# Optimization experiments

Hardware: AMD Instinct MI355X
Metric: run time of the kernel (lower is better)

The kernel has to match this reference:

```python
import jax, jax.numpy as jnp
import numpy as np

HEADS = 4
DIM_HEAD = 32
TOPK_RATIO = 0.25
MIN_TOPK = 32
QKEEP_RATIO = 0.75
MIN_QKEEP = 64
LN_EPS = 1e-5


def _ln(x, g, b):
    m = x.mean(-1, keepdims=True)
    v = x.var(-1, keepdims=True)  # biased, matches torch LayerNorm
    return (x - m) / jnp.sqrt(v + LN_EPS) * g + b


def setup_inputs() -> dict:
    key = jax.random.key(0)
    ks = jax.random.split(key, 8)
    b, n, x, y, w, d = 4, 4, 8, 8, 8, 128
    hd = HEADS * DIM_HEAD  # 128
    shape = (b, n, x, y, w, w, d)
    inp = {
        'q': jax.random.normal(ks[0], shape, jnp.float32),
        'k': jax.random.normal(ks[1], shape, jnp.float32),
        'v': jax.random.normal(ks[2], shape, jnp.float32),
        'ln_q_g': jnp.ones((d,), jnp.float32), 'ln_q_b': jnp.zeros((d,), jnp.float32),
        'ln_k_g': jnp.ones((d,), jnp.float32), 'ln_k_b': jnp.zeros((d,), jnp.float32),
        'ln_v_g': jnp.ones((d,), jnp.float32), 'ln_v_b': jnp.zeros((d,), jnp.float32),
        'wq': 0.02 * jax.random.normal(ks[3], (d, hd), jnp.float32), 'bq': jnp.zeros((hd,), jnp.float32),
        'wk': 0.02 * jax.random.normal(ks[4], (d, hd), jnp.float32), 'bk': jnp.zeros((hd,), jnp.float32),
        'wv': 0.02 * jax.random.normal(ks[5], (d, hd), jnp.float32), 'bv': jnp.zeros((hd,), jnp.float32),
        'w_proj': 0.02 * jax.random.normal(ks[6], (hd, d), jnp.float32), 'b_proj': jnp.zeros((d,), jnp.float32),
    }
    return inp


def _forward(q, k, v, ln_q_g, ln_q_b, ln_k_g, ln_k_b, ln_v_g, ln_v_b,
             wq, bq, wk, bk, wv, bv, w_proj, b_proj):
    b, n, xH, yW, w1, w2, d = q.shape
    H, Dh = HEADS, DIM_HEAD

    def towin(t):  # b n x y w1 w2 d -> b (x y) (n w1 w2) d
        tb, tn, tx, ty, t1, t2, td = t.shape
        return t.transpose(0, 2, 3, 1, 4, 5, 6).reshape(tb, tx * ty, tn * t1 * t2, td)

    qw = _ln(towin(q), ln_q_g, ln_q_b) @ wq + bq
    kw = _ln(towin(k), ln_k_g, ln_k_b) @ wk + bk
    vw = _ln(towin(v), ln_v_g, ln_v_b) @ wv + bv

    def heads(t):  # b l q (h d) -> (b h) l q d
        B, L, N, _ = t.shape
        return t.reshape(B, L, N, H, Dh).transpose(0, 3, 1, 2, 4).reshape(B * H, L, N, Dh)

    qh, kh, vh = heads(qw), heads(kw), heads(vw)
    BH, L, Q, _ = qh.shape

    # dynamic query saliency pruning
    keep_q = min(max(max(int(Q * QKEEP_RATIO), MIN_QKEEP), 1), Q)
    sal = jnp.sum(qh * qh, axis=-1)  # (BH, L, Q)
    qidx = jax.lax.top_k(sal, keep_q)[1]
    qmask = jnp.zeros(sal.shape, bool).at[
        jnp.arange(BH)[:, None, None], jnp.arange(L)[None, :, None], qidx].set(True)
    qh = qh * qmask[..., None]

    scale = Dh ** -0.5
    logits = jnp.einsum('blqd,blkd->blqk', qh * scale, kh)  # (BH, L, Q, K)
    K = logits.shape[-1]

    # per-query top-k key masking
    topk = min(max(int(K * TOPK_RATIO), MIN_TOPK), K)
    kidx = jax.lax.top_k(logits, topk)[1]
    kmask = jnp.zeros(logits.shape, bool).at[
        jnp.arange(BH)[:, None, None, None], jnp.arange(L)[None, :, None, None],
        jnp.arange(Q)[None, None, :, None], kidx].set(True)
    logits = jnp.where(kmask, logits, -jnp.inf)
    att = jax.nn.softmax(logits, axis=-1)

    a = jnp.einsum('blqk,blkd->blqd', att, vh)
    # (b h) l (n w1 w2) d -> b n x y w1 w2 (h d)
    a = a.reshape(b, H, L, n, w1, w2, Dh).transpose(0, 3, 2, 4, 5, 6, 1, 7) if False else a
    a = jnp.einsum('...->...', a)  # no-op placeholder removed below
    a = att  # placeholder
    raise RuntimeError


def reference(q, k, v, ln_q_g, ln_q_b, ln_k_g, ln_k_b, ln_v_g, ln_v_b,
              wq, bq, wk, bk, wv, bv, w_proj, b_proj):
    b, n, xH, yW, w1, w2, d = q.shape
    H, Dh = HEADS, DIM_HEAD

    def towin(t):  # b n x y w1 w2 d -> b (x y) (n w1 w2) d
        tb, tn, tx, ty, t1, t2, td = t.shape
        return t.transpose(0, 2, 3, 1, 4, 5, 6).reshape(tb, tx * ty, tn * t1 * t2, td)

    qw = _ln(towin(q), ln_q_g, ln_q_b) @ wq + bq
    kw = _ln(towin(k), ln_k_g, ln_k_b) @ wk + bk
    vw = _ln(towin(v), ln_v_g, ln_v_b) @ wv + bv

    def heads(t):  # b l q (h d) -> (b h) l q d
        B, L, N, _ = t.shape
        return t.reshape(B, L, N, H, Dh).transpose(0, 3, 1, 2, 4).reshape(B * H, L, N, Dh)

    qh, kh, vh = heads(qw), heads(kw), heads(vw)
    BH, L, Q, _ = qh.shape

    keep_q = min(max(max(int(Q * QKEEP_RATIO), MIN_QKEEP), 1), Q)
    sal = jnp.sum(qh * qh, axis=-1)  # (BH, L, Q)
    qidx = jax.lax.top_k(sal, keep_q)[1]
    qmask = jnp.zeros(sal.shape, bool).at[
        jnp.arange(BH)[:, None, None], jnp.arange(L)[None, :, None], qidx].set(True)
    qh = qh * qmask[..., None]

    scale = Dh ** -0.5
    logits = jnp.einsum('blqd,blkd->blqk', qh * scale, kh)  # (BH, L, Q, K)
    K = logits.shape[-1]

    topk = min(max(int(K * TOPK_RATIO), MIN_TOPK), K)
    kidx = jax.lax.top_k(logits, topk)[1]
    kmask = jnp.zeros(logits.shape, bool).at[
        jnp.arange(BH)[:, None, None, None], jnp.arange(L)[None, :, None, None],
        jnp.arange(Q)[None, None, :, None], kidx].set(True)
    logits = jnp.where(kmask, logits, -jnp.inf)
    att = jax.nn.softmax(logits, axis=-1)

    a = jnp.einsum('blqk,blkd->blqd', att, vh)
    # (b h) l (n w1 w2) dh -> b n l w1 w2 (h dh) -> b n x y w1 w2 hd
    a = a.reshape(b, H, L, n, w1, w2, Dh).transpose(0, 3, 2, 4, 5, 1, 6)
    a = a.reshape(b, n, xH, yW, w1, w2, H * Dh)
    z = a @ w_proj + b_proj
    return z.mean(axis=1)
```

## Files before the change

### kernel.cpp

```cpp
#include <hip/hip_runtime.h>
#include <stdint.h>

#define LN_EPS 1e-5f
#define SCALE 0.17677669529663687f
#define KEEPQ 192

typedef __attribute__((ext_vector_type(8))) short short8v;
typedef __attribute__((ext_vector_type(4))) float float4v;

__device__ __forceinline__ short f2bf(float x) {
  uint32_t u = __float_as_uint(x);
  uint32_t r = (u + 0x7FFFu + ((u >> 16) & 1u)) >> 16;
  return (short)r;
}
__device__ __forceinline__ float bf2f(short s) {
  return __uint_as_float(((uint32_t)(uint16_t)s) << 16);
}
__device__ __forceinline__ uint32_t pk2(short a, short b) {
  return (uint32_t)(uint16_t)a | ((uint32_t)(uint16_t)b << 16);
}
__device__ __forceinline__ void split3(float x, short &h, short &m, short &l) {
  h = f2bf(x); float r1 = x - bf2f(h);
  m = f2bf(r1); float r2 = r1 - bf2f(m);
  l = f2bf(r2);
}
__device__ __forceinline__ uint32_t fmap(float x) {
  uint32_t bb = __float_as_uint(x);
  if ((bb & 0x7FFFFFFFu) == 0u) bb = 0u;
  return (bb & 0x80000000u) ? ~bb : (bb | 0x80000000u);
}
__device__ __forceinline__ float unmap(uint32_t m) {
  uint32_t b = (m & 0x80000000u) ? (m & 0x7FFFFFFFu) : ~m;
  return __uint_as_float(b);
}

__device__ __forceinline__ void topk_sel(const float v[4], int k, int lane, bool sel[4]) {
  uint32_t u[4];
  #pragma unroll
  for (int s = 0; s < 4; ++s) u[s] = fmap(v[s]);
  uint32_t prefix = 0u;
  bool exact = false;
  for (int bit = 31; bit >= 0; --bit) {
    uint32_t cand = prefix | (1u << bit);
    int c = 0;
    #pragma unroll
    for (int s = 0; s < 4; ++s) c += __popcll(__ballot(u[s] >= cand));
    if (c >= k) {
      prefix = cand;
      if (c == k) { exact = true; break; }
    }
  }
  if (exact) {
    #pragma unroll
    for (int s = 0; s < 4; ++s) sel[s] = (u[s] >= prefix);
    return;
  }
  const uint32_t T = prefix;
  int gt = 0;
  unsigned long long eb[4];
  #pragma unroll
  for (int s = 0; s < 4; ++s) {
    gt += __popcll(__ballot(u[s] > T));
    eb[s] = __ballot(u[s] == T);
  }
  const int need = k - gt;
  const unsigned long long lm = (1ull << lane) - 1ull;
  int base = 0;
  #pragma unroll
  for (int s = 0; s < 4; ++s) {
    int before = base + __popcll(eb[s] & lm);
    sel[s] = (u[s] > T) || ((u[s] == T) && (before < need));
    base += __popcll(eb[s]);
  }
}

__global__ __launch_bounds__(256) void k_lnproj(
    const float* __restrict__ xq, const float* __restrict__ xk, const float* __restrict__ xv,
    const float* __restrict__ gq, const float* __restrict__ beq,
    const float* __restrict__ gk, const float* __restrict__ bek,
    const float* __restrict__ gv, const float* __restrict__ bev,
    const float* __restrict__ wq, const float* __restrict__ biq,
    const float* __restrict__ wk, const float* __restrict__ bik,
    const float* __restrict__ wv, const float* __restrict__ biv,
    float* __restrict__ qh, short* __restrict__ k0, short* __restrict__ k1,
    short* __restrict__ k2, short* __restrict__ vt)
{
  __shared__ float xs[64 * 132];
  const int tile = blockIdx.x;
  const int t = blockIdx.y;
  const float* x  = (t == 0) ? xq : (t == 1) ? xk : xv;
  const float* g  = (t == 0) ? gq : (t == 1) ? gk : gv;
  const float* be = (t == 0) ? beq : (t == 1) ? bek : bev;
  const float* W  = (t == 0) ? wq : (t == 1) ? wk : wv;
  const float* bi = (t == 0) ? biq : (t == 1) ? bik : biv;
  const int tid = threadIdx.x;

  const float4* xg = (const float4*)(x + (size_t)tile * 64 * 128);
  #pragma unroll
  for (int i = 0; i < 8; ++i) {
    int idx = tid + i * 256;
    int r = idx >> 5;
    int c = (idx & 31) * 4;
    *(float4*)&xs[r * 132 + c] = xg[idx];
  }
  __syncthreads();

  {
    int r = tid >> 2, p = tid & 3;
    float s = 0.f, sq = 0.f;
    #pragma unroll
    for (int c = 0; c < 32; ++c) {
      float vv = xs[r * 132 + p * 32 + c];
      s += vv; sq += vv * vv;
    }
    s += __shfl_xor(s, 1, 64); sq += __shfl_xor(sq, 1, 64);
    s += __shfl_xor(s, 2, 64); sq += __shfl_xor(sq, 2, 64);
    float mean = s * (1.0f / 128.0f);
    float var = sq * (1.0f / 128.0f) - mean * mean;
    float rstd = rsqrtf(var + LN_EPS);
    #pragma unroll
    for (int c = 0; c < 32; ++c) {
      int cc = p * 32 + c;
      xs[r * 132 + cc] = (xs[r * 132 + cc] - mean) * rstd * g[cc] + be[cc];
    }
  }
  __syncthreads();

  const int ty = tid >> 4, tx = tid & 15;
  float acc[4][8];
  #pragma unroll
  for (int i = 0; i < 4; ++i)
    #pragma unroll
    for (int j = 0; j < 8; ++j) acc[i][j] = 0.f;

  #pragma unroll 2
  for (int kk = 0; kk < 128; kk += 4) {
    float aa[4][4];
    #pragma unroll
    for (int i = 0; i < 4; ++i)
      *(float4*)&aa[i][0] = *(const float4*)&xs[(ty * 4 + i) * 132 + kk];
    #pragma unroll
    for (int t2 = 0; t2 < 4; ++t2) {
      const float4 w0 = *(const float4*)&W[(kk + t2) * 128 + tx * 8];
      const float4 w1 = *(const float4*)&W[(kk + t2) * 128 + tx * 8 + 4];
      #pragma unroll
      for (int i = 0; i < 4; ++i) {
        acc[i][0] = fmaf(aa[i][t2], w0.x, acc[i][0]);
        acc[i][1] = fmaf(aa[i][t2], w0.y, acc[i][1]);
        acc[i][2] = fmaf(aa[i][t2], w0.z, acc[i][2]);
        acc[i][3] = fmaf(aa[i][t2], w0.w, acc[i][3]);
        acc[i][4] = fmaf(aa[i][t2], w1.x, acc[i][4]);
        acc[i][5] = fmaf(aa[i][t2], w1.y, acc[i][5]);
        acc[i][6] = fmaf(aa[i][t2], w1.z, acc[i][6]);
        acc[i][7] = fmaf(aa[i][t2], w1.w, acc[i][7]);
      }
    }
  }

  float bias[8];
  #pragma unroll
  for (int j = 0; j < 8; ++j) bias[j] = bi[tx * 8 + j];
  const int b  = tile >> 8;
  const int n  = (tile >> 6) & 3;
  const int l  = ((tile >> 3) & 7) * 8 + (tile & 7);
  const int h  = tx >> 2;
  const int dh0 = (tx & 3) * 8;
  const size_t win = (size_t)(b * 4 + h) * 64 + l;

  if (t == 0) {
    #pragma unroll
    for (int i = 0; i < 4; ++i) {
      int j = n * 64 + ty * 4 + i;
      size_t off = (win * 256 + j) * 32 + dh0;
      float4 o0 = make_float4(acc[i][0] + bias[0], acc[i][1] + bias[1],
                              acc[i][2] + bias[2], acc[i][3] + bias[3]);
      float4 o1 = make_float4(acc[i][4] + bias[4], acc[i][5] + bias[5],
                              acc[i][6] + bias[6], acc[i][7] + bias[7]);
      *(float4*)&qh[off] = o0;
      *(float4*)&qh[off + 4] = o1;
    }
  } else if (t == 1) {
    #pragma unroll
    for (int i = 0; i < 4; ++i) {
      int j = n * 64 + ty * 4 + i;
      size_t off = (win * 256 + j) * 32 + dh0;
      short hh[8], mm[8], ll[8];
      #pragma unroll
      for (int jj = 0; jj < 8; ++jj) {
        float o = acc[i][jj] + bias[jj];
        split3(o, hh[jj], mm[jj], ll[jj]);
      }
      *(uint4*)&k0[off] = make_uint4(pk2(hh[0], hh[1]), pk2(hh[2], hh[3]),
                                     pk2(hh[4], hh[5]), pk2(hh[6], hh[7]));
      *(uint4*)&k1[off] = make_uint4(pk2(mm[0], mm[1]), pk2(mm[2], mm[3]),
                                     pk2(mm[4], mm[5]), pk2(mm[6], mm[7]));
      *(uint4*)&k2[off] = make_uint4(pk2(ll[0], ll[1]), pk2(ll[2], ll[3]),
                                     pk2(ll[4], ll[5]), pk2(ll[6], ll[7]));
    }
  } else {
    short vb[4][8];
    #pragma unroll
    for (int i = 0; i < 4; ++i)
      #pragma unroll
      for (int jj = 0; jj < 8; ++jj)
        vb[i][jj] = f2bf(acc[i][jj] + bias[jj]);
    const int jbase = n * 64 + ty * 4;
    #pragma unroll
    for (int jj = 0; jj < 8; ++jj) {
      size_t off = (win * 32 + dh0 + jj) * 256 + jbase;
      *(uint2*)&vt[off] = make_uint2(pk2(vb[0][jj], vb[1][jj]),
                                     pk2(vb[2][jj], vb[3][jj]));
    }
  }
}

__global__ __launch_bounds__(256, 2) void k_attn(
    const float* __restrict__ qh, const short* __restrict__ k0,
    const short* __restrict__ k1, const short* __restrict__ k2,
    const short* __restrict__ vt, float* __restrict__ abar)
{
  __shared__ __align__(16) short ks0s[256][36];
  __shared__ __align__(16) short ks1s[256][36];
  __shared__ __align__(16) short vts[32][264];
  __shared__ __align__(16) short pt[4][16][72];
  __shared__ float sal[256];
  __shared__ float keepf[256];

  const int win = blockIdx.x;
  const int bh = win >> 6, l = win & 63;
  const int b = bh >> 2, h = bh & 3;
  const int tid = threadIdx.x;
  const int lane = tid & 63, wv = tid >> 6;
  const int g = lane >> 4, p = lane & 15;
  const int wt = wv;

  const float* qw = qh + (size_t)win * 8192;
  const short* kw2 = k2 + (size_t)win * 8192;

  {
    const uint4* s0 = (const uint4*)(k0 + (size_t)win * 8192);
    const uint4* s1 = (const uint4*)(k1 + (size_t)win * 8192);
    const uint4* sv = (const uint4*)(vt + (size_t)win * 8192);
    #pragma unroll
    for (int i = 0; i < 4; ++i) {
      int ci = tid + i * 256;
      int r = ci >> 2, c8 = (ci & 3) * 8;
      *(uint4*)&ks0s[r][c8] = s0[ci];
      *(uint4*)&ks1s[r][c8] = s1[ci];
      int rv = ci >> 5, c16 = (ci & 31) * 8;
      *(uint4*)&vts[rv][c16] = sv[ci];
    }
  }
  {
    const float4* qg2 = (const float4*)(qw + (size_t)tid * 32);
    float ss = 0.f;
    #pragma unroll
    for (int i = 0; i < 8; ++i) {
      float4 vv = qg2[i];
      ss += vv.x * vv.x + vv.y * vv.y + vv.z * vv.z + vv.w * vv.w;
    }
    sal[tid] = ss;
  }
  __syncthreads();
  if (wv == 0) {
    float v[4]; bool selq[4];
    #pragma unroll
    for (int s = 0; s < 4; ++s) v[s] = sal[lane + 64 * s];
    topk_sel(v, KEEPQ, lane, selq);
    #pragma unroll
    for (int s = 0; s < 4; ++s) keepf[lane + 64 * s] = selq[s] ? SCALE : 0.0f;
  }
  __syncthreads();

  float4v pacc0 = {0.f, 0.f, 0.f, 0.f};
  float4v pacc1 = {0.f, 0.f, 0.f, 0.f};
  short* ptw = &pt[wv][0][0];

  for (int n = 0; n < 4; ++n) {
    const int qbase = n * 64 + wt * 16;
    const float kfp = keepf[qbase + p];
    const bool kept = (kfp != 0.0f);

    short8v aq0, aq1, aq2;
    {
      const float* qrow = qw + (size_t)(qbase + p) * 32 + g * 8;
      float4 qa = *(const float4*)qrow;
      float4 qb = *(const float4*)(qrow + 4);
      float qv[8] = {qa.x, qa.y, qa.z, qa.w, qb.x, qb.y, qb.z, qb.w};
      #pragma unroll
      for (int e = 0; e < 8; ++e) {
        short hh, mm, ll;
        split3(qv[e] * kfp, hh, mm, ll);
        aq0[e] = hh; aq1[e] = mm; aq2[e] = ll;
      }
    }

    float4v acc[16];
    #pragma unroll
    for (int c = 0; c < 16; ++c) {
      const short8v b0 = *(const short8v*)&ks0s[c * 16 + p][g * 8];
      const short8v b1 = *(const short8v*)&ks1s[c * 16 + p][g * 8];
      const short8v b2 = *(const short8v*)(kw2 + (size_t)(c * 16 + p) * 32 + g * 8);
      float4v a = {0.f, 0.f, 0.f, 0.f};
      a = __builtin_amdgcn_mfma_f32_16x16x32_bf16(b0, aq0, a, 0, 0, 0);
      a = __builtin_amdgcn_mfma_f32_16x16x32_bf16(b0, aq1, a, 0, 0, 0);
      a = __builtin_amdgcn_mfma_f32_16x16x32_bf16(b0, aq2, a, 0, 0, 0);
      a = __builtin_amdgcn_mfma_f32_16x16x32_bf16(b1, aq0, a, 0, 0, 0);
      a = __builtin_amdgcn_mfma_f32_16x16x32_bf16(b1, aq1, a, 0, 0, 0);
      a = __builtin_amdgcn_mfma_f32_16x16x32_bf16(b2, aq0, a, 0, 0, 0);
      acc[c] = a;
    }

    float fmx = acc[0][0], fmn = acc[0][0];
    #pragma unroll
    for (int c = 0; c < 16; ++c) {
      #pragma unroll
      for (int r = 0; r < 4; ++r) {
        fmx = fmaxf(fmx, acc[c][r]);
        fmn = fminf(fmn, acc[c][r]);
      }
    }
    fmx = fmaxf(fmx, __shfl_xor(fmx, 16));
    fmn = fminf(fmn, __shfl_xor(fmn, 16));
    fmx = fmaxf(fmx, __shfl_xor(fmx, 32));
    fmn = fminf(fmn, __shfl_xor(fmn, 32));
    const uint32_t umaxu = fmap(fmx), uminu = fmap(fmn);
    const float fm = unmap(umaxu);

    uint32_t piv = 0u; int cnt = 256; int sb = -1; bool bdone = true;
    if (kept) {
      uint32_t du = umaxu ^ uminu;
      if (du != 0u) {
        sb = 31 - __clz(du);
        piv = (sb >= 31) ? 0u : (umaxu & (0xFFFFFFFFu << (sb + 1)));
        bdone = false;
      } else { piv = umaxu; }
    }
    for (int bit = 31; bit >= 0; --bit) {
      if (__all(bdone)) break;
      const uint32_t cand = piv | (1u << bit);
      const float tf = unmap(cand);
      int cc = 0;
      #pragma unroll
      for (int c = 0; c < 16; ++c) {
        #pragma unroll
        for (int r = 0; r < 4; ++r) cc += (acc[c][r] >= tf) ? 1 : 0;
      }
      cc += __shfl_xor(cc, 16);
      cc += __shfl_xor(cc, 32);
      if (!bdone && bit <= sb && cc >= 64) {
        piv = cand; cnt = cc;
        if (cc == 64) bdone = true;
      }
    }
    const float Tf = unmap(piv);

    uint64_t selm = 0ull;
    if (kept) {
      if (cnt == 64) {
        #pragma unroll
        for (int c = 0; c < 16; ++c)
          #pragma unroll
          for (int r = 0; r < 4; ++r)
            selm |= (acc[c][r] >= Tf) ? (1ull << (4 * c + r)) : 0ull;
      } else {
        int gtc = 0;
        #pragma unroll
        for (int c = 0; c < 16; ++c)
          #pragma unroll
          for (int r = 0; r < 4; ++r) gtc += (acc[c][r] > Tf) ? 1 : 0;
        gtc += __shfl_xor(gtc, 16);
        gtc += __shfl_xor(gtc, 32);
        const int need = 64 - gtc;
        uint64_t em = 0ull;
        #pragma unroll
        for (int c = 0; c < 16; ++c)
          #pragma unroll
          for (int r = 0; r < 4; ++r)
            em |= (acc[c][r] == Tf) ? (1ull << (4 * c + r)) : 0ull;
        uint64_t emA = __shfl_xor((unsigned long long)em, 16);
        uint64_t emB = __shfl_xor((unsigned long long)em, 32);
        uint64_t emC = __shfl_xor((unsigned long long)emA, 32);
        uint64_t M0 = (g == 0) ? em : ((g == 1) ? emA : ((g == 2) ? emB : emC));
        uint64_t M1 = (g == 1) ? em : ((g == 0) ? emA : ((g == 3) ? emB : emC));
        uint64_t M2 = (g == 2) ? em : ((g == 3) ? emA : ((g == 0) ? emB : emC));
        uint64_t M3 = (g == 3) ? em : ((g == 2) ? emA : ((g == 1) ? emB : emC));
        int pref = 0;
        #pragma unroll
        for (int c = 0; c < 16; ++c) {
          int n0 = (int)((M0 >> (4 * c)) & 15ull);
          int n1 = (int)((M1 >> (4 * c)) & 15ull);
          int n2 = (int)((M2 >> (4 * c)) & 15ull);
          int n3 = (int)((M3 >> (4 * c)) & 15ull);
          int gs = ((g > 0) ? __popc(n0) : 0) + ((g > 1) ? __popc(n1) : 0)
                 + ((g > 2) ? __popc(n2) : 0);
          int on = (int)((em >> (4 * c)) & 15ull);
          #pragma unroll
          for (int r = 0; r < 4; ++r) {
            bool s2;
            if (acc[c][r] > Tf) s2 = true;
            else if (acc[c][r] == Tf) {
              int before = pref + gs + __popc(on & ((1 << r) - 1));
              s2 = (before < need);
            } else s2 = false;
            selm |= s2 ? (1ull << (4 * c + r)) : 0ull;
          }
          pref += __popc(n0) + __popc(n1) + __popc(n2) + __popc(n3);
        }
      }
    }

    float esum = 0.f;
    #pragma unroll
    for (int c = 0; c < 16; ++c) {
      #pragma unroll
      for (int r = 0; r < 4; ++r) {
        float e;
        if (kept)
          e = ((selm >> (4 * c + r)) & 1ull) ? __expf(acc[c][r] - fm) : 0.0f;
        else
          e = (c < 4) ? 0.015625f : 0.0f;
        acc[c][r] = e;
        esum += e;
      }
    }
    esum += __shfl_xor(esum, 16);
    esum += __shfl_xor(esum, 32);
    const float inv = kept ? (1.0f / esum) : 1.0f;

    #pragma unroll
    for (int t = 0; t < 4; ++t) {
      #pragma unroll
      for (int kq = 0; kq < 2; ++kq) {
        const int kk = 2 * t + kq;
        const int ce = 2 * kk, co = ce + 1;
        uint2 w0 = make_uint2(pk2(f2bf(acc[ce][0] * inv), f2bf(acc[ce][1] * inv)),
                              pk2(f2bf(acc[ce][2] * inv), f2bf(acc[ce][3] * inv)));
        uint2 w1 = make_uint2(pk2(f2bf(acc[co][0] * inv), f2bf(acc[co][1] * inv)),
                              pk2(f2bf(acc[co][2] * inv), f2bf(acc[co][3] * inv)));
        *(uint2*)&ptw[p * 72 + kq * 32 + 4 * g] = w0;
        *(uint2*)&ptw[p * 72 + kq * 32 + 16 + 4 * g] = w1;
      }
      asm volatile("s_waitcnt lgkmcnt(0)" ::: "memory");
      __builtin_amdgcn_sched_barrier(0);
      #pragma unroll
      for (int kq = 0; kq < 2; ++kq) {
        const int kk = 2 * t + kq;
        short8v pa = *(const short8v*)&ptw[p * 72 + kq * 32 + 8 * g];
        short8v v0 = *(const short8v*)&vts[p][kk * 32 + 8 * g];
        short8v v1 = *(const short8v*)&vts[16 + p][kk * 32 + 8 * g];
        pacc0 = __builtin_amdgcn_mfma_f32_16x16x32_bf16(pa, v0, pacc0, 0, 0, 0);
        pacc1 = __builtin_amdgcn_mfma_f32_16x16x32_bf16(pa, v1, pacc1, 0, 0, 0);
      }
    }
  }

  #pragma unroll
  for (int rr = 0; rr < 4; ++rr) {
    const int w = wt * 16 + g * 4 + rr;
    size_t o = ((size_t)(b * 64 + l) * 64 + w) * 128 + h * 32;
    abar[o + p] = pacc0[rr] * 0.25f;
    abar[o + 16 + p] = pacc1[rr] * 0.25f;
  }
}

__global__ __launch_bounds__(256) void k_proj(
    const float* __restrict__ abar, const float* __restrict__ W,
    const float* __restrict__ bi, float* __restrict__ out)
{
  __shared__ float xs[64 * 132];
  const int tile = blockIdx.x;
  const int tid = threadIdx.x;
  const float4* xg = (const float4*)(abar + (size_t)tile * 64 * 128);
  #pragma unroll
  for (int i = 0; i < 8; ++i) {
    int idx = tid + i * 256;
    int r = idx >> 5, c = (idx & 31) * 4;
    *(float4*)&xs[r * 132 + c] = xg[idx];
  }
  __syncthreads();

  const int ty = tid >> 4, tx = tid & 15;
  float acc[4][8];
  #pragma unroll
  for (int i = 0; i < 4; ++i)
    #pragma unroll
    for (int j = 0; j < 8; ++j) acc[i][j] = 0.f;

  #pragma unroll 2
  for (int kk = 0; kk < 128; kk += 4) {
    float aa[4][4];
    #pragma unroll
    for (int i = 0; i < 4; ++i)
      *(float4*)&aa[i][0] = *(const float4*)&xs[(ty * 4 + i) * 132 + kk];
    #pragma unroll
    for (int t2 = 0; t2 < 4; ++t2) {
      const float4 w0 = *(const float4*)&W[(kk + t2) * 128 + tx * 8];
      const float4 w1 = *(const float4*)&W[(kk + t2) * 128 + tx * 8 + 4];
      #pragma unroll
      for (int i = 0; i < 4; ++i) {
        acc[i][0] = fmaf(aa[i][t2], w0.x, acc[i][0]);
        acc[i][1] = fmaf(aa[i][t2], w0.y, acc[i][1]);
        acc[i][2] = fmaf(aa[i][t2], w0.z, acc[i][2]);
        acc[i][3] = fmaf(aa[i][t2], w0.w, acc[i][3]);
        acc[i][4] = fmaf(aa[i][t2], w1.x, acc[i][4]);
        acc[i][5] = fmaf(aa[i][t2], w1.y, acc[i][5]);
        acc[i][6] = fmaf(aa[i][t2], w1.z, acc[i][6]);
        acc[i][7] = fmaf(aa[i][t2], w1.w, acc[i][7]);
      }
    }
  }
  #pragma unroll
  for (int i = 0; i < 4; ++i) {
    size_t row = (size_t)tile * 64 + ty * 4 + i;
    float4 o0 = make_float4(acc[i][0] + bi[tx * 8 + 0], acc[i][1] + bi[tx * 8 + 1],
                            acc[i][2] + bi[tx * 8 + 2], acc[i][3] + bi[tx * 8 + 3]);
    float4 o1 = make_float4(acc[i][4] + bi[tx * 8 + 4], acc[i][5] + bi[tx * 8 + 5],
                            acc[i][6] + bi[tx * 8 + 6], acc[i][7] + bi[tx * 8 + 7]);
    *(float4*)&out[row * 128 + tx * 8] = o0;
    *(float4*)&out[row * 128 + tx * 8 + 4] = o1;
  }
}

extern "C" void kernel_launch(void* const* d_in, const int* in_sizes, int n_in,
                              void* d_out, int out_size, void* d_ws, size_t ws_size,
                              hipStream_t stream) {
  (void)in_sizes; (void)n_in; (void)out_size; (void)ws_size;
  const float* xq   = (const float*)d_in[0];
  const float* xk   = (const float*)d_in[1];
  const float* xv   = (const float*)d_in[2];
  const float* gq   = (const float*)d_in[3];
  const float* beq  = (const float*)d_in[4];
  const float* gk   = (const float*)d_in[5];
  const float* bek  = (const float*)d_in[6];
  const float* gv   = (const float*)d_in[7];
  const float* bev  = (const float*)d_in[8];
  const float* wq   = (const float*)d_in[9];
  const float* biq  = (const float*)d_in[10];
  const float* wk   = (const float*)d_in[11];
  const float* bik  = (const float*)d_in[12];
  const float* wv   = (const float*)d_in[13];
  const float* biv  = (const float*)d_in[14];
  const float* wpr  = (const float*)d_in[15];
  const float* bpr  = (const float*)d_in[16];

  char* ws = (char*)d_ws;
  float* qh  = (float*)(ws);
  short* k0  = (short*)(ws + 33554432);
  short* k1  = (short*)(ws + 50331648);
  short* k2  = (short*)(ws + 67108864);
  short* vt  = (short*)(ws + 83886080);
  float* abar = (float*)(ws + 100663296);

  k_lnproj<<<dim3(1024, 3), 256, 0, stream>>>(xq, xk, xv, gq, beq, gk, bek, gv, bev,
                                              wq, biq, wk, bik, wv, biv,
                                              qh, k0, k1, k2, vt);
  k_attn<<<1024, 256, 0, stream>>>(qh, k0, k1, k2, vt, abar);
  k_proj<<<256, 256, 0, stream>>>(abar, wpr, bpr, (float*)d_out);
}
```

Baseline: 370.6 us.

## Cut LDS use for occupancy 3 and run 16-bit radix top-k select

Drops the second K split from shared memory and reads it from global instead, then raises launch bounds to three blocks per SM. The top-k threshold search now runs on 16-bit truncated keys packed two per register, so it needs at most 16 radix passes instead of 32. Ties at the truncated threshold are resolved by an iterative argmax over the full-precision values. This trades extra global traffic, a possibly long tie-resolution loop and tighter register limits for more occupancy and cheaper selection.

```diff
diff --git a/kernel.cpp b/kernel.cpp
--- a/kernel.cpp
+++ b/kernel.cpp
@@ -214,13 +214,12 @@
   }
 }
 
-__global__ __launch_bounds__(256, 2) void k_attn(
+__global__ __launch_bounds__(256, 3) void k_attn(
     const float* __restrict__ qh, const short* __restrict__ k0,
     const short* __restrict__ k1, const short* __restrict__ k2,
     const short* __restrict__ vt, float* __restrict__ abar)
 {
   __shared__ __align__(16) short ks0s[256][36];
-  __shared__ __align__(16) short ks1s[256][36];
   __shared__ __align__(16) short vts[32][264];
   __shared__ __align__(16) short pt[4][16][72];
   __shared__ float sal[256];
@@ -235,20 +234,17 @@
   const int wt = wv;
 
   const float* qw = qh + (size_t)win * 8192;
+  const short* kw1 = k1 + (size_t)win * 8192;
   const short* kw2 = k2 + (size_t)win * 8192;
 
   {
     const uint4* s0 = (const uint4*)(k0 + (size_t)win * 8192);
-    const uint4* s1 = (const uint4*)(k1 + (size_t)win * 8192);
     const uint4* sv = (const uint4*)(vt + (size_t)win * 8192);
     #pragma unroll
     for (int i = 0; i < 4; ++i) {
       int ci = tid + i * 256;
-      int r = ci >> 2, c8 = (ci & 3) * 8;
-      *(uint4*)&ks0s[r][c8] = s0[ci];
-      *(uint4*)&ks1s[r][c8] = s1[ci];
-      int rv = ci >> 5, c16 = (ci & 31) * 8;
-      *(uint4*)&vts[rv][c16] = sv[ci];
+      *(uint4*)&ks0s[ci >> 2][(ci & 3) * 8] = s0[ci];
+      *(uint4*)&vts[ci >> 5][(ci & 31) * 8] = sv[ci];
     }
   }
   {
@@ -299,7 +295,7 @@
     #pragma unroll
     for (int c = 0; c < 16; ++c) {
       const short8v b0 = *(const short8v*)&ks0s[c * 16 + p][g * 8];
-      const short8v b1 = *(const short8v*)&ks1s[c * 16 + p][g * 8];
+      const short8v b1 = *(const short8v*)(kw1 + (size_t)(c * 16 + p) * 32 + g * 8);
       const short8v b2 = *(const short8v*)(kw2 + (size_t)(c * 16 + p) * 32 + g * 8);
       float4v a = {0.f, 0.f, 0.f, 0.f};
       a = __builtin_amdgcn_mfma_f32_16x16x32_bf16(b0, aq0, a, 0, 0, 0);
@@ -324,91 +320,94 @@
     fmn = fminf(fmn, __shfl_xor(fmn, 16));
     fmx = fmaxf(fmx, __shfl_xor(fmx, 32));
     fmn = fminf(fmn, __shfl_xor(fmn, 32));
-    const uint32_t umaxu = fmap(fmx), uminu = fmap(fmn);
-    const float fm = unmap(umaxu);
-
-    uint32_t piv = 0u; int cnt = 256; int sb = -1; bool bdone = true;
+    const uint32_t umax32 = fmap(fmx), umin32 = fmap(fmn);
+    const float fm = unmap(umax32);
+
+    uint32_t kp[32];
+    #pragma unroll
+    for (int j = 0; j < 32; ++j) {
+      const int e0 = 2 * j, e1 = 2 * j + 1;
+      uint32_t lo = fmap(acc[e0 >> 2][e0 & 3]) >> 16;
+      uint32_t hi = fmap(acc[e1 >> 2][e1 & 3]) >> 16;
+      kp[j] = lo | (hi << 16);
+    }
+
+    const uint32_t t16max = umax32 >> 16, t16min = umin32 >> 16;
+    uint32_t piv = 0u; int cntge = 256; bool bdone = true;
     if (kept) {
-      uint32_t du = umaxu ^ uminu;
-      if (du != 0u) {
-        sb = 31 - __clz(du);
-        piv = (sb >= 31) ? 0u : (umaxu & (0xFFFFFFFFu << (sb + 1)));
+      uint32_t du = t16max ^ t16min;
+      if (du == 0u) { piv = t16max; }
+      else {
+        int sb = 31 - __clz(du);
+        piv = t16max & ~((2u << sb) - 1u);
         bdone = false;
-      } else { piv = umaxu; }
-    }
-    for (int bit = 31; bit >= 0; --bit) {
+      }
+    }
+    for (int bit = 15; bit >= 0; --bit) {
       if (__all(bdone)) break;
       const uint32_t cand = piv | (1u << bit);
-      const float tf = unmap(cand);
       int cc = 0;
       #pragma unroll
-      for (int c = 0; c < 16; ++c) {
-        #pragma unroll
-        for (int r = 0; r < 4; ++r) cc += (acc[c][r] >= tf) ? 1 : 0;
+      for (int j = 0; j < 32; ++j) {
+        cc += ((kp[j] & 0xFFFFu) >= cand) ? 1 : 0;
+        cc += ((kp[j] >> 16) >= cand) ? 1 : 0;
       }
       cc += __shfl_xor(cc, 16);
       cc += __shfl_xor(cc, 32);
-      if (!bdone && bit <= sb && cc >= 64) {
-        piv = cand; cnt = cc;
+      if (!bdone && cc >= 64) {
+        piv = cand; cntge = cc;
         if (cc == 64) bdone = true;
       }
     }
-    const float Tf = unmap(piv);
-
-    uint64_t selm = 0ull;
+    const uint32_t T16 = piv;
+
+    uint64_t gtm = 0ull, eqm = 0ull, picked = 0ull;
+    int need = 0;
     if (kept) {
-      if (cnt == 64) {
+      #pragma unroll
+      for (int j = 0; j < 32; ++j) {
+        const uint32_t lo = kp[j] & 0xFFFFu, hi = kp[j] >> 16;
+        gtm |= (lo > T16) ? (1ull << (2 * j)) : 0ull;
+        eqm |= (lo == T16) ? (1ull << (2 * j)) : 0ull;
+        gtm |= (hi > T16) ? (1ull << (2 * j + 1)) : 0ull;
+        eqm |= (hi == T16) ? (1ull << (2 * j + 1)) : 0ull;
+      }
+      if (cntge != 64) {
+        int gp = (int)__popcll(gtm);
+        gp += __shfl_xor(gp, 16);
+        gp += __shfl_xor(gp, 32);
+        need = 64 - gp;
+      }
+    }
+
+    for (int it = 0; it < 64; ++it) {
+      if (__all(need <= 0)) break;
+      uint32_t best = 0u; int bk = 256;
+      if (need > 0) {
         #pragma unroll
-        for (int c = 0; c < 16; ++c)
-          #pragma unroll
-          for (int r = 0; r < 4; ++r)
-            selm |= (acc[c][r] >= Tf) ? (1ull << (4 * c + r)) : 0ull;
-      } else {
-        int gtc = 0;
-        #pragma unroll
-        for (int c = 0; c < 16; ++c)
-          #pragma unroll
-          for (int r = 0; r < 4; ++r) gtc += (acc[c][r] > Tf) ? 1 : 0;
-        gtc += __shfl_xor(gtc, 16);
-        gtc += __shfl_xor(gtc, 32);
-        const int need = 64 - gtc;
-        uint64_t em = 0ull;
-        #pragma unroll
-        for (int c = 0; c < 16; ++c)
-          #pragma unroll
-          for (int r = 0; r < 4; ++r)
-            em |= (acc[c][r] == Tf) ? (1ull << (4 * c + r)) : 0ull;
-        uint64_t emA = __shfl_xor((unsigned long long)em, 16);
-        uint64_t emB = __shfl_xor((unsigned long long)em, 32);
-        uint64_t emC = __shfl_xor((unsigned long long)emA, 32);
-        uint64_t M0 = (g == 0) ? em : ((g == 1) ? emA : ((g == 2) ? emB : emC));
-        uint64_t M1 = (g == 1) ? em : ((g == 0) ? emA : ((g == 3) ? emB : emC));
-        uint64_t M2 = (g == 2) ? em : ((g == 3) ? emA : ((g == 0) ? emB : emC));
-        uint64_t M3 = (g == 3) ? em : ((g == 2) ? emA : ((g == 1) ? emB : emC));
-        int pref = 0;
-        #pragma unroll
-        for (int c = 0; c < 16; ++c) {
-          int n0 = (int)((M0 >> (4 * c)) & 15ull);
-          int n1 = (int)((M1 >> (4 * c)) & 15ull);
-          int n2 = (int)((M2 >> (4 * c)) & 15ull);
-          int n3 = (int)((M3 >> (4 * c)) & 15ull);
-          int gs = ((g > 0) ? __popc(n0) : 0) + ((g > 1) ? __popc(n1) : 0)
-                 + ((g > 2) ? __popc(n2) : 0);
-          int on = (int)((em >> (4 * c)) & 15ull);
-          #pragma unroll
-          for (int r = 0; r < 4; ++r) {
-            bool s2;
-            if (acc[c][r] > Tf) s2 = true;
-            else if (acc[c][r] == Tf) {
-              int before = pref + gs + __popc(on & ((1 << r) - 1));
-              s2 = (before < need);
-            } else s2 = false;
-            selm |= s2 ? (1ull << (4 * c + r)) : 0ull;
+        for (int e = 0; e < 64; ++e) {
+          if (((eqm >> e) & 1ull) && !((picked >> e) & 1ull)) {
+            const uint32_t f = fmap(acc[e >> 2][e & 3]);
+            const int gk = ((e >> 2) << 4) | (g << 2) | (e & 3);
+            if (f > best || (f == best && gk < bk)) { best = f; bk = gk; }
           }
-          pref += __popc(n0) + __popc(n1) + __popc(n2) + __popc(n3);
         }
       }
-    }
+      #pragma unroll
+      for (int d = 16; d <= 32; d <<= 1) {
+        const uint32_t ov = (uint32_t)__shfl_xor((int)best, d);
+        const int oi = __shfl_xor(bk, d);
+        if (ov > best || (ov == best && oi < bk)) { best = ov; bk = oi; }
+      }
+      if (need > 0) {
+        if (((bk >> 2) & 3) == g) {
+          const int e = ((bk >> 4) << 2) | (bk & 3);
+          picked |= (1ull << e);
+        }
+        need -= 1;
+      }
+    }
+    const uint64_t selm = kept ? (gtm | ((cntge == 64) ? eqm : picked)) : 0ull;
 
     float esum = 0.f;
     #pragma unroll
```

Measured after the change: 445.9 us. 20.3% more time.
